# Performance work log

Hardware: AMD Instinct MI355X
Metric: run time of the kernel (lower is better)

## Reference

```python
import jax, jax.numpy as jnp
import numpy as np

IN_FEATURES = 4096
OUT_FEATURES = 11008
BATCH, SEQ = 4, 2048


def setup_inputs() -> dict:
    key = jax.random.key(0)
    k_x, k_w, k_b = jax.random.split(key, 3)
    x = jax.random.normal(k_x, (BATCH, SEQ, IN_FEATURES), dtype=jnp.float32)
    # int8-valued quantized weight (stored int32 for portability; values in [-127,127])
    weight_int8 = jax.random.randint(k_w, (OUT_FEATURES, IN_FEATURES), -127, 128, dtype=jnp.int32)
    # per-tensor symmetric quantization scale (max|w|/127 in original; any positive scalar)
    scale = jnp.float32(0.01)
    bias = jax.random.normal(k_b, (OUT_FEATURES,), dtype=jnp.float32) * 0.02
    return {"x": x, "weight_int8": weight_int8, "scale": scale, "bias": bias}


def reference(x, weight_int8, scale, bias):
    # Codec is lossless: decompress() yields the int8 tensor exactly, then
    # dequantizes: w = int8.astype(float) * scale; forward is F.linear(x, w, bias).
    w = weight_int8.astype(jnp.float32) * scale  # [out, in]
    # x: [b, s, in] @ w.T -> [b, s, out]
    return jnp.einsum("bsi,oi->bso", x, w) + bias
```

## Files before the change

### kernel.cpp

```cpp
#include <hip/hip_runtime.h>
#include <stdint.h>


#define M_DIM 8192
#define N_DIM 11008
#define K_DIM 4096

#define BM 256
#define BN 256
#define BK 32
#define NT (K_DIM / BK)
#define NBN (N_DIM / BN)
#define NBM (M_DIM / BM)
#define GRID (NBM * NBN)

typedef short bf16x8 __attribute__((ext_vector_type(8)));
typedef float f32x4 __attribute__((ext_vector_type(4)));

__device__ __forceinline__ unsigned short f2bf(float f) {
    union { float f; uint32_t u; } c; c.f = f;
    uint32_t u = c.u;
    return (unsigned short)((u + 0x7FFFu + ((u >> 16) & 1u)) >> 16);
}

__global__ __launch_bounds__(256) void cvt_fused_kernel(
    const float* __restrict__ x, const int* __restrict__ w,
    unsigned short* __restrict__ xo, unsigned short* __restrict__ wo)
{
    const int NX4 = M_DIM * K_DIM / 4;
    const int NW4 = N_DIM * K_DIM / 4;
    const int stride = gridDim.x * blockDim.x;
    const int t0 = blockIdx.x * blockDim.x + threadIdx.x;
    for (int i = t0; i < NX4; i += stride) {
        float4 v = ((const float4*)x)[i];
        ushort4 r;
        r.x = f2bf(v.x); r.y = f2bf(v.y); r.z = f2bf(v.z); r.w = f2bf(v.w);
        ((ushort4*)xo)[i] = r;
    }
    for (int i = t0; i < NW4; i += stride) {
        int4 v = ((const int4*)w)[i];
        ushort4 r;
        r.x = f2bf((float)v.x); r.y = f2bf((float)v.y);
        r.z = f2bf((float)v.z); r.w = f2bf((float)v.w);
        ((ushort4*)wo)[i] = r;
    }
}

__device__ __forceinline__ void async16(const void* g, void* l) {
    __builtin_amdgcn_global_load_lds((__attribute__((address_space(1))) void*)g,
                                     (__attribute__((address_space(3))) void*)l,
                                     16, 0, 0);
}


__global__ __launch_bounds__(512, 2) void gemm_bf16_kernel(
    const unsigned short* __restrict__ A,
    const unsigned short* __restrict__ B,
    const float* __restrict__ scale_p,
    const float* __restrict__ bias,
    float* __restrict__ out)
{
    __shared__ __attribute__((aligned(16))) char lds[131072];

    const int t    = threadIdx.x;
    const int lane = t & 63;
    const int w    = t >> 6;
    const int wm   = w >> 2;
    const int wn   = w & 3;
    const int quad = lane >> 4;
    const int l16  = lane & 15;

    const int bid = blockIdx.x;
    const int swz = (bid & 7) * (GRID / 8) + (bid >> 3);
    const int bm = swz / NBN;
    const int bn = swz % NBN;

    f32x4 acc[8][4];
#pragma unroll
    for (int i = 0; i < 8; i++)
#pragma unroll
        for (int j = 0; j < 4; j++)
            acc[i][j] = (f32x4){0.f, 0.f, 0.f, 0.f};

    const int rowh = t >> 2;
    const int slot = t & 3;
    const int csw  = ((slot ^ ((rowh >> 1) & 3)) << 4);
    const char* aS0 = (const char*)(A + (size_t)(bm * BM + rowh) * K_DIM) + csw;
    const char* bS0 = (const char*)(B + (size_t)(bn * BN + rowh) * K_DIM) + csw;
    const char* aS1 = aS0 + (size_t)128 * K_DIM * 2;
    const char* bS1 = bS0 + (size_t)128 * K_DIM * 2;
    char* aD = lds + t * 16;
    char* bD = lds + 65536 + t * 16;

#define STAGE(buf, kt) do { \
        const size_t kb_ = (size_t)(kt) * (BK * 2); \
        async16(aS0 + kb_, aD + ((buf) << 14)); \
        async16(aS1 + kb_, aD + ((buf) << 14) + 8192); \
        async16(bS0 + kb_, bD + ((buf) << 14)); \
        async16(bS1 + kb_, bD + ((buf) << 14) + 8192); \
    } while (0)

    STAGE(0, 0); STAGE(1, 1); STAGE(2, 2);

    const int coff = ((quad ^ ((l16 >> 1) & 3)) << 4);
    const int aoff = (wm * 128 + l16) * (BK * 2) + coff;
    const int boff = 65536 + (wn * 64 + l16) * (BK * 2) + coff;

#pragma unroll 4
    for (int kt = 0; kt < NT; kt++) {
        STAGE((kt + 3) & 3, (kt + 3) & (NT - 1));

        asm volatile("s_waitcnt vmcnt(12)" ::: "memory");
        __builtin_amdgcn_s_barrier();
        asm volatile("" ::: "memory");

        const char* Ab = lds + ((kt & 3) << 14) + aoff;
        const char* Bb = lds + ((kt & 3) << 14) + boff;

        bf16x8 bfr[4], afr[4];
#pragma unroll
        for (int j = 0; j < 4; j++)
            bfr[j] = *(const bf16x8*)(Bb + j * 1024);
#pragma unroll
        for (int i = 0; i < 4; i++)
            afr[i] = *(const bf16x8*)(Ab + i * 1024);

        __builtin_amdgcn_s_setprio(1);
#pragma unroll
        for (int i = 0; i < 4; i++)
#pragma unroll
            for (int j = 0; j < 4; j++)
                acc[i][j] = __builtin_amdgcn_mfma_f32_16x16x32_bf16(
                    afr[i], bfr[j], acc[i][j], 0, 0, 0);
        __builtin_amdgcn_s_setprio(0);

#pragma unroll
        for (int i = 0; i < 4; i++)
            afr[i] = *(const bf16x8*)(Ab + (i + 4) * 1024);

        __builtin_amdgcn_s_setprio(1);
#pragma unroll
        for (int i = 0; i < 4; i++)
#pragma unroll
            for (int j = 0; j < 4; j++)
                acc[i + 4][j] = __builtin_amdgcn_mfma_f32_16x16x32_bf16(
                    afr[i], bfr[j], acc[i + 4][j], 0, 0, 0);
        __builtin_amdgcn_s_setprio(0);

        asm volatile("s_waitcnt lgkmcnt(0)" ::: "memory");
        __builtin_amdgcn_s_barrier();
    }
#undef STAGE

    const float scale = *scale_p;
    const int gcol = bn * BN + wn * 64 + l16;
    float bvals[4];
#pragma unroll
    for (int j = 0; j < 4; j++) bvals[j] = bias[gcol + j * 16];

#pragma unroll
    for (int i = 0; i < 8; i++) {
        const int grow0 = bm * BM + wm * 128 + i * 16 + quad * 4;
#pragma unroll
        for (int r = 0; r < 4; r++) {
            float* orow = out + (size_t)(grow0 + r) * N_DIM + gcol;
#pragma unroll
            for (int j = 0; j < 4; j++)
                orow[j * 16] = acc[i][j][r] * scale + bvals[j];
        }
    }
}

__global__ __launch_bounds__(256) void naive_kernel(
    const float* __restrict__ x, const int* __restrict__ w8,
    const float* __restrict__ scale_p, const float* __restrict__ bias,
    float* __restrict__ out)
{
    size_t idx = (size_t)blockIdx.x * 256 + threadIdx.x;
    if (idx >= (size_t)M_DIM * N_DIM) return;
    int n = (int)(idx % N_DIM);
    size_t m = idx / N_DIM;
    const float* xr = x + m * K_DIM;
    const int* wr = w8 + (size_t)n * K_DIM;
    float acc = 0.f;
    for (int k = 0; k < K_DIM; k++) acc += xr[k] * (float)wr[k];
    out[idx] = acc * (*scale_p) + bias[n];
}

extern "C" void kernel_launch(void* const* d_in, const int* in_sizes, int n_in,
                              void* d_out, int out_size, void* d_ws, size_t ws_size,
                              hipStream_t stream) {
    const float* x     = (const float*)d_in[0];
    const int*   w8    = (const int*)d_in[1];
    const float* scale = (const float*)d_in[2];
    const float* bias  = (const float*)d_in[3];
    float* out = (float*)d_out;

    const size_t a_bytes = (size_t)M_DIM * K_DIM * 2;
    const size_t b_bytes = (size_t)N_DIM * K_DIM * 2;

    if (ws_size >= a_bytes + b_bytes) {
        unsigned short* a_bf = (unsigned short*)d_ws;
        unsigned short* b_bf = (unsigned short*)((char*)d_ws + a_bytes);
        cvt_fused_kernel<<<2048, 256, 0, stream>>>(x, w8, a_bf, b_bf);
        gemm_bf16_kernel<<<GRID, 512, 0, stream>>>(a_bf, b_bf, scale, bias, out);
    } else {
        size_t total = (size_t)M_DIM * N_DIM;
        naive_kernel<<<(unsigned)((total + 255) / 256), 256, 0, stream>>>(
            x, w8, scale, bias, out);
    }
}
```

Before: 1.228 ms.

## Double-buffer GEMM LDS fragments in registers and drop per-iteration trailing barrier

The GEMM main loop now preloads the A and B fragments for the next k-tile into a second register set while MFMAs consume the current set. The two loop bodies alternate roles, so each iteration needs only one barrier instead of two, and the vmcnt wait is tightened so the next buffer is resident before it is read. This is meant to hide LDS read latency behind MFMA work and cut synchronisation overhead. In exchange it raises VGPR pressure and narrows the global prefetch slack by one stage. The conversion kernel also switches its input loads to nontemporal loads to reduce cache pollution.

```diff
diff --git a/kernel.cpp b/kernel.cpp
--- a/kernel.cpp
+++ b/kernel.cpp
@@ -16,6 +16,9 @@
 
 typedef short bf16x8 __attribute__((ext_vector_type(8)));
 typedef float f32x4 __attribute__((ext_vector_type(4)));
+typedef float fvec4 __attribute__((ext_vector_type(4)));
+typedef int   ivec4 __attribute__((ext_vector_type(4)));
+typedef unsigned short usvec4 __attribute__((ext_vector_type(4)));
 
 __device__ __forceinline__ unsigned short f2bf(float f) {
     union { float f; uint32_t u; } c; c.f = f;
@@ -32,17 +35,17 @@
     const int stride = gridDim.x * blockDim.x;
     const int t0 = blockIdx.x * blockDim.x + threadIdx.x;
     for (int i = t0; i < NX4; i += stride) {
-        float4 v = ((const float4*)x)[i];
-        ushort4 r;
+        fvec4 v = __builtin_nontemporal_load(&((const fvec4*)x)[i]);
+        usvec4 r;
         r.x = f2bf(v.x); r.y = f2bf(v.y); r.z = f2bf(v.z); r.w = f2bf(v.w);
-        ((ushort4*)xo)[i] = r;
+        ((usvec4*)xo)[i] = r;
     }
     for (int i = t0; i < NW4; i += stride) {
-        int4 v = ((const int4*)w)[i];
-        ushort4 r;
+        ivec4 v = __builtin_nontemporal_load(&((const ivec4*)w)[i]);
+        usvec4 r;
         r.x = f2bf((float)v.x); r.y = f2bf((float)v.y);
         r.z = f2bf((float)v.z); r.w = f2bf((float)v.w);
-        ((ushort4*)wo)[i] = r;
+        ((usvec4*)wo)[i] = r;
     }
 }
 
@@ -100,55 +103,48 @@
         async16(bS1 + kb_, bD + ((buf) << 14) + 8192); \
     } while (0)
 
-    STAGE(0, 0); STAGE(1, 1); STAGE(2, 2);
-
     const int coff = ((quad ^ ((l16 >> 1) & 3)) << 4);
     const int aoff = (wm * 128 + l16) * (BK * 2) + coff;
     const int boff = 65536 + (wn * 64 + l16) * (BK * 2) + coff;
 
-#pragma unroll 4
-    for (int kt = 0; kt < NT; kt++) {
+    bf16x8 fa[8], fb[4], ga[8], gb[4];
+
+    STAGE(0, 0); STAGE(1, 1); STAGE(2, 2);
+    asm volatile("s_waitcnt vmcnt(8)" ::: "memory");
+    __builtin_amdgcn_s_barrier();
+    asm volatile("" ::: "memory");
+#pragma unroll
+    for (int j = 0; j < 4; j++) fb[j] = *(const bf16x8*)(lds + boff + j * 1024);
+#pragma unroll
+    for (int i = 0; i < 8; i++) fa[i] = *(const bf16x8*)(lds + aoff + i * 1024);
+
+    auto body = [&](int kt, bf16x8 (&ca)[8], bf16x8 (&cb)[4],
+                    bf16x8 (&na)[8], bf16x8 (&nb)[4]) __attribute__((always_inline)) {
         STAGE((kt + 3) & 3, (kt + 3) & (NT - 1));
-
-        asm volatile("s_waitcnt vmcnt(12)" ::: "memory");
+        asm volatile("s_waitcnt vmcnt(8)" ::: "memory");
         __builtin_amdgcn_s_barrier();
         asm volatile("" ::: "memory");
 
-        const char* Ab = lds + ((kt & 3) << 14) + aoff;
-        const char* Bb = lds + ((kt & 3) << 14) + boff;
-
-        bf16x8 bfr[4], afr[4];
-#pragma unroll
-        for (int j = 0; j < 4; j++)
-            bfr[j] = *(const bf16x8*)(Bb + j * 1024);
-#pragma unroll
-        for (int i = 0; i < 4; i++)
-            afr[i] = *(const bf16x8*)(Ab + i * 1024);
+        const char* Abn = lds + (((kt + 1) & 3) << 14) + aoff;
+        const char* Bbn = lds + (((kt + 1) & 3) << 14) + boff;
+#pragma unroll
+        for (int j = 0; j < 4; j++) nb[j] = *(const bf16x8*)(Bbn + j * 1024);
+#pragma unroll
+        for (int i = 0; i < 8; i++) na[i] = *(const bf16x8*)(Abn + i * 1024);
 
         __builtin_amdgcn_s_setprio(1);
 #pragma unroll
-        for (int i = 0; i < 4; i++)
+        for (int i = 0; i < 8; i++)
 #pragma unroll
             for (int j = 0; j < 4; j++)
                 acc[i][j] = __builtin_amdgcn_mfma_f32_16x16x32_bf16(
-                    afr[i], bfr[j], acc[i][j], 0, 0, 0);
+                    ca[i], cb[j], acc[i][j], 0, 0, 0);
         __builtin_amdgcn_s_setprio(0);
-
-#pragma unroll
-        for (int i = 0; i < 4; i++)
-            afr[i] = *(const bf16x8*)(Ab + (i + 4) * 1024);
-
-        __builtin_amdgcn_s_setprio(1);
-#pragma unroll
-        for (int i = 0; i < 4; i++)
-#pragma unroll
-            for (int j = 0; j < 4; j++)
-                acc[i + 4][j] = __builtin_amdgcn_mfma_f32_16x16x32_bf16(
-                    afr[i], bfr[j], acc[i + 4][j], 0, 0, 0);
-        __builtin_amdgcn_s_setprio(0);
-
-        asm volatile("s_waitcnt lgkmcnt(0)" ::: "memory");
-        __builtin_amdgcn_s_barrier();
+    };
+
+    for (int kt = 0; kt < NT; kt += 2) {
+        body(kt,     fa, fb, ga, gb);
+        body(kt + 1, ga, gb, fa, fb);
     }
 #undef STAGE
 
```

After: 1.182 ms. -3.7%, faster.
